# Optimization experiments

Measured on AMD Instinct MI355X. Metric: run time of the kernel, lower is better.

## Reference

```python
import jax, jax.numpy as jnp
import numpy as np

N_HEADS = 16
EPSILON = 0.01
SCORE_SCALE = 1.0
C_CONST = 2.0 + EPSILON


def setup_inputs() -> dict:
    key = jax.random.key(0)
    k1, k2, k3 = jax.random.split(key, 3)
    B, T, D = 2, 2048, 1024
    x = jax.random.normal(k1, (B, T, D), dtype=jnp.float32)
    # torch nn.Linear convention: weight [out_features, in_features], y = x @ W.T
    Wqkv = jax.random.normal(k2, (3 * D, D), dtype=jnp.float32) * (1.0 / np.sqrt(D))
    Wout = jax.random.normal(k3, (D, D), dtype=jnp.float32) * (1.0 / np.sqrt(D))
    return {"x": x, "Wqkv": Wqkv, "Wout": Wout}


def reference(x, Wqkv, Wout):
    B, T, D = x.shape
    H = N_HEADS
    hd = D // H
    qkv = x @ Wqkv.T  # [B, T, 3D]
    q, k, v = jnp.split(qkv, 3, axis=-1)
    # [B, H, T, hd]
    q = q.reshape(B, T, H, hd).transpose(0, 2, 1, 3).astype(jnp.float32)
    k = k.reshape(B, T, H, hd).transpose(0, 2, 1, 3).astype(jnp.float32)
    v = v.reshape(B, T, H, hd).transpose(0, 2, 1, 3).astype(jnp.float32)
    # L2 normalize along head dim (F.normalize uses eps=1e-12 via clamp of norm)
    qn = q / jnp.maximum(jnp.linalg.norm(q, axis=-1, keepdims=True), 1e-12)
    kn = k / jnp.maximum(jnp.linalg.norm(k, axis=-1, keepdims=True), 1e-12)
    # full T x T kernel matrix per (batch, head)
    x_dot = jnp.einsum("bhtd,bhsd->bhts", qn, kn)
    denom = jnp.maximum(C_CONST - 2.0 * x_dot, 1e-6)
    K = (x_dot * x_dot) / denom * SCORE_SCALE
    causal = jnp.tril(jnp.ones((T, T), dtype=bool))  # keep lower triangle incl. diag
    K = jnp.where(causal[None, None, :, :], K, 0.0)
    numerator = jnp.einsum("bhts,bhsd->bhtd", K, v)
    denominator = jnp.sum(K, axis=-1, keepdims=True)
    out = numerator / (denominator + 1e-6)
    out = out.transpose(0, 2, 1, 3).reshape(B, T, D)
    return out @ Wout.T
```

## Files before the change

kernel.cpp:

```cpp
#include <hip/hip_runtime.h>
#include <hip/hip_bf16.h>

#define T_SEQ 2048
#define D_MODEL 1024
#define BT 4096
#define QKV_N 3072

typedef __attribute__((ext_vector_type(8))) short bf16x8;
typedef __attribute__((ext_vector_type(4))) short bf16x4;
typedef __attribute__((ext_vector_type(4))) float f32x4;

typedef unsigned int __attribute__((address_space(1))) as1_uint;
typedef unsigned int __attribute__((address_space(3))) as3_uint;

__device__ __forceinline__ unsigned short f2bf(float f) {
    unsigned u = __builtin_bit_cast(unsigned, f);
    u += 0x7fffu + ((u >> 16) & 1u);
    return (unsigned short)(u >> 16);
}
__device__ __forceinline__ float bf2f(unsigned short h) {
    unsigned u = ((unsigned)h) << 16;
    return __builtin_bit_cast(float, u);
}
__device__ __forceinline__ void gload_lds16(const void* g, void* l) {
    __builtin_amdgcn_global_load_lds((const as1_uint*)g, (as3_uint*)l, 16, 0, 0);
}
__device__ __forceinline__ unsigned cvtpk_bf16(float lo, float hi) {
    unsigned r;
    asm("v_cvt_pk_bf16_f32 %0, %1, %2" : "=v"(r) : "v"(lo), "v"(hi));
    return r;
}

__global__ __launch_bounds__(256) void cvt_bf16_3(const float* __restrict__ s0, unsigned short* __restrict__ d0, int n0,
                                                  const float* __restrict__ s1, unsigned short* __restrict__ d1, int n1,
                                                  const float* __restrict__ s2, unsigned short* __restrict__ d2, int n2) {
    int i = blockIdx.x * 256 + threadIdx.x;
    const float* s; unsigned short* d;
    if (i < n0) { s = s0; d = d0; }
    else if (i < n0 + n1) { i -= n0; s = s1; d = d1; }
    else if (i < n0 + n1 + n2) { i -= n0 + n1; s = s2; d = d2; }
    else return;
    const float4* sp = (const float4*)s + (size_t)i * 2;
    const float4 a = sp[0], b = sp[1];
    uint4 o;
    o.x = (unsigned)f2bf(a.x) | ((unsigned)f2bf(a.y) << 16);
    o.y = (unsigned)f2bf(a.z) | ((unsigned)f2bf(a.w) << 16);
    o.z = (unsigned)f2bf(b.x) | ((unsigned)f2bf(b.y) << 16);
    o.w = (unsigned)f2bf(b.z) | ((unsigned)f2bf(b.w) << 16);
    ((uint4*)d)[i] = o;
}

template<int MODE>
__global__ __launch_bounds__(256) void gemm_bt_mfma(const unsigned short* __restrict__ A,
                                                    const unsigned short* __restrict__ B,
                                                    void* __restrict__ Cout,
                                                    unsigned short* __restrict__ qbp,
                                                    unsigned short* __restrict__ kbp,
                                                    int M, int N, int K) {
    __shared__ unsigned short As[128 * 64];
    __shared__ unsigned short Bs[128 * 64];
    const int tid = threadIdx.x;
    const int w = tid >> 6;
    const int l = tid & 63;
    const int l15 = l & 15, l4 = l >> 4;

    const int nblocks = (M / 128) * (N / 128);
    const int cpx = nblocks >> 3;
    const int id2 = (blockIdx.x & 7) * cpx + (blockIdx.x >> 3);
    const int bm = (id2 & 31) * 128;
    const int bn = (id2 >> 5) * 128;

    const int wm = (w >> 1) * 64, wn = (w & 1) * 64;

    const f32x4 z = {0.f, 0.f, 0.f, 0.f};
    f32x4 acc[4][4];
#pragma unroll
    for (int m = 0; m < 4; ++m)
#pragma unroll
        for (int n = 0; n < 4; ++n) acc[m][n] = z;

    const int lrow = l >> 3;
    const int lslot = (l & 7) ^ (lrow & 7);

    for (int k0 = 0; k0 < K; k0 += 64) {
#pragma unroll
        for (int i = 0; i < 4; ++i) {
            const int row = w * 32 + i * 8 + lrow;
            gload_lds16(A + (size_t)(bm + row) * K + k0 + lslot * 8, As + (w * 4 + i) * 512);
            gload_lds16(B + (size_t)(bn + row) * K + k0 + lslot * 8, Bs + (w * 4 + i) * 512);
        }
        __syncthreads();
        bf16x8 af[4][2], bfr[4][2];
#pragma unroll
        for (int m = 0; m < 4; ++m) {
            const int row = wm + m * 16 + l15;
            af[m][0] = *(const bf16x8*)(As + row * 64 + ((l4 ^ (row & 7)) * 8));
            af[m][1] = *(const bf16x8*)(As + row * 64 + (((4 + l4) ^ (row & 7)) * 8));
        }
#pragma unroll
        for (int n = 0; n < 4; ++n) {
            const int row = wn + n * 16 + l15;
            bfr[n][0] = *(const bf16x8*)(Bs + row * 64 + ((l4 ^ (row & 7)) * 8));
            bfr[n][1] = *(const bf16x8*)(Bs + row * 64 + (((4 + l4) ^ (row & 7)) * 8));
        }
#pragma unroll
        for (int m = 0; m < 4; ++m)
#pragma unroll
            for (int n = 0; n < 4; ++n) {
                acc[m][n] = __builtin_amdgcn_mfma_f32_16x16x32_bf16(af[m][0], bfr[n][0], acc[m][n], 0, 0, 0);
                acc[m][n] = __builtin_amdgcn_mfma_f32_16x16x32_bf16(af[m][1], bfr[n][1], acc[m][n], 0, 0, 0);
            }
        __syncthreads();
    }

    if (MODE == 0) {
#pragma unroll
        for (int m = 0; m < 4; ++m)
#pragma unroll
            for (int n = 0; n < 4; ++n)
#pragma unroll
                for (int r = 0; r < 4; ++r) {
                    const int row = bm + wm + m * 16 + l4 * 4 + r;
                    const int col = bn + wn + n * 16 + l15;
                    ((float*)Cout)[(size_t)row * N + col] = acc[m][n][r];
                }
    } else {
        const int gcol0 = bn + wn;
        const int part = gcol0 >> 10;
        const int h = (gcol0 >> 6) & 15;
        if (part < 2) {
            unsigned short* dst = part ? kbp : qbp;
#pragma unroll
            for (int m = 0; m < 4; ++m)
#pragma unroll
                for (int r = 0; r < 4; ++r) {
                    float ss = 0.f;
#pragma unroll
                    for (int n = 0; n < 4; ++n) ss = fmaf(acc[m][n][r], acc[m][n][r], ss);
                    ss += __shfl_xor(ss, 1);
                    ss += __shfl_xor(ss, 2);
                    ss += __shfl_xor(ss, 4);
                    ss += __shfl_xor(ss, 8);
                    const float sc = 1.0f / fmaxf(sqrtf(ss), 1e-12f);
                    const int row = bm + wm + m * 16 + l4 * 4 + r;
                    const int bh2 = (row >> 11) * 16 + h;
                    unsigned short* pdst = dst + ((size_t)bh2 * T_SEQ + (row & 2047)) * 64 + l15;
#pragma unroll
                    for (int n = 0; n < 4; ++n) pdst[n * 16] = f2bf(acc[m][n][r] * sc);
                }
        } else {
            unsigned short* vrow = (unsigned short*)Cout;
            const int vcol0 = gcol0 - 2048;
#pragma unroll
            for (int m = 0; m < 4; ++m)
#pragma unroll
                for (int n = 0; n < 4; ++n)
#pragma unroll
                    for (int r = 0; r < 4; ++r) {
                        const int row = bm + wm + m * 16 + l4 * 4 + r;
                        vrow[(size_t)row * D_MODEL + vcol0 + n * 16 + l15] = f2bf(acc[m][n][r]);
                    }
        }
    }
}

__global__ __launch_bounds__(256) void v_cvt_T(const unsigned short* __restrict__ vrow,
                                               unsigned short* __restrict__ vbT) {
    __shared__ unsigned short tile[64][72];
    const int bh = blockIdx.y;
    const int b = bh >> 4, h = bh & 15;
    const int t0 = blockIdx.x * 64;
    const int r = threadIdx.x >> 2;
    const int c = (threadIdx.x & 3) * 16;
    const unsigned short* src = vrow + (size_t)(b * T_SEQ + t0 + r) * D_MODEL + h * 64 + c;
    uint4 v0 = *(const uint4*)(src);
    uint4 v1 = *(const uint4*)(src + 8);
    unsigned short tmp[16];
    *(uint4*)tmp = v0;
    *(uint4*)(tmp + 8) = v1;
#pragma unroll
    for (int j = 0; j < 16; ++j) tile[c + j][r] = tmp[j];
    __syncthreads();
    const int d = threadIdx.x >> 2;
    const int tc = (threadIdx.x & 3) * 16;
    const int t5 = tc >> 5, t4 = (tc >> 4) & 1;
    unsigned short* dstrow = vbT + ((size_t)bh * 64 + d) * T_SEQ + t0;
    const int dp = d & 7;
#pragma unroll
    for (int q = 0; q < 4; ++q) {
        unsigned short tmp2[4];
#pragma unroll
        for (int i = 0; i < 4; ++i) tmp2[i] = tile[d][tc + q * 4 + i];
        const int slot = (t5 * 4 + q) ^ dp;
        *(uint2*)(dstrow + slot * 8 + t4 * 4) = *(uint2*)tmp2;
    }
}

#define AT_TS 64

static __device__ const unsigned char task_tab[48] = {
    (15<<1)|0,(16<<1)|0,(17<<1)|0,(18<<1)|0,(19<<1)|0,(20<<1)|0,(21<<1)|0,(22<<1)|0,
    (23<<1)|0,(24<<1)|0,(25<<1)|0,(26<<1)|0,(27<<1)|0,(28<<1)|0,(29<<1)|0,(30<<1)|0,
    (31<<1)|0,(31<<1)|1,
    (14<<1)|0,(30<<1)|1,(13<<1)|0,(29<<1)|1,(12<<1)|0,(28<<1)|1,(11<<1)|0,(27<<1)|1,
    (10<<1)|0,(26<<1)|1,(9<<1)|0,(25<<1)|1,(8<<1)|0,(24<<1)|1,(7<<1)|0,(23<<1)|1,
    (6<<1)|0,(22<<1)|1,(5<<1)|0,(21<<1)|1,(4<<1)|0,(20<<1)|1,(3<<1)|0,(19<<1)|1,
    (2<<1)|0,(18<<1)|1,(1<<1)|0,(17<<1)|1,(0<<1)|0,(16<<1)|1,
};

__global__ __launch_bounds__(256, 4) void attn_mfma(const unsigned short* __restrict__ qb,
                                                    const unsigned short* __restrict__ kb,
                                                    const unsigned short* __restrict__ vbT,
                                                    unsigned short* __restrict__ attnb,
                                                    unsigned short* __restrict__ pnum,
                                                    float* __restrict__ pden) {
    __shared__ unsigned short Ks[2][64 * 64];
    __shared__ unsigned short Vs[2][64 * 64];

    const int tid = threadIdx.x;
    const int w = tid >> 6;
    const int l = tid & 63;
    const int l15 = l & 15, l4 = l >> 4;

    const int id = blockIdx.x;
    const int xcd = id & 7;
    const int wq = id >> 3;
    const int hl = wq & 3;
    const int task = wq >> 2;
    const int bh = xcd * 4 + hl;
    const int tv = task_tab[task];
    const int j = tv >> 1;
    const int chunk = tv & 1;
    const int nst = chunk ? (j - 15) : (j < 16 ? j + 1 : 16);
    const bool mfin = chunk ? true : (j < 16);
    const int s_base = chunk * 16;
    const int t0 = j * 64;

    const size_t hb = (size_t)bh * T_SEQ * 64;

    const int lrow = l >> 3;
    const int lslot = (l & 7) ^ (lrow & 7);
    const unsigned short* kgp[2];
    const unsigned short* vgp[2];
    unsigned short* kdst[2];
    unsigned short* vdst[2];
#pragma unroll
    for (int c = 0; c < 2; ++c) {
        const int row = w * 16 + c * 8 + lrow;
        kgp[c] = kb + hb + (size_t)(s_base * 64 + row) * 64 + lslot * 8;
        vgp[c] = vbT + hb + (size_t)row * T_SEQ + s_base * 64 + (l & 7) * 8;
        kdst[c] = &Ks[0][(w * 2 + c) * 512];
        vdst[c] = &Vs[0][(w * 2 + c) * 512];
    }

    const int p = l15 & 7;
    const unsigned short* kfp0 = &Ks[0][0] + l15 * 64 + ((l4 ^ p) * 8);
    const unsigned short* kfp1 = &Ks[0][0] + l15 * 64 + (((4 + l4) ^ p) * 8);
    const unsigned short* vfp0 = &Vs[0][0] + l15 * 64 + ((l4 ^ p) * 8);
    const unsigned short* vfp1 = &Vs[0][0] + l15 * 64 + (((4 + l4) ^ p) * 8);

    bf16x8 qf0, qf1;
    {
        const unsigned short* qp = qb + hb + (size_t)(t0 + w * 16 + l15) * 64 + l4 * 8;
        qf0 = *(const bf16x8*)(qp);
        qf1 = *(const bf16x8*)(qp + 32);
    }

    const f32x4 z = {0.f, 0.f, 0.f, 0.f};
    f32x4 acc[4];
#pragma unroll
    for (int i = 0; i < 4; ++i) acc[i] = z;
    float accd = 0.f;

    const int wrow0 = t0 + w * 16;
    const int tq = wrow0 + l15;

#pragma unroll
    for (int c = 0; c < 2; ++c) {
        gload_lds16(kgp[c], kdst[c]);
        gload_lds16(vgp[c], vdst[c]);
    }

    auto compute_tile = [&](int roff, int s0, bool mask) {
        const unsigned short* kc0 = kfp0 + roff;
        const unsigned short* kc1 = kfp1 + roff;
        f32x4 sC[4];
        __builtin_amdgcn_s_setprio(1);
#pragma unroll
        for (int sf = 0; sf < 4; ++sf) {
            bf16x8 kf0 = *(const bf16x8*)(kc0 + sf * 1024);
            bf16x8 kf1 = *(const bf16x8*)(kc1 + sf * 1024);
            f32x4 c = z;
            c = __builtin_amdgcn_mfma_f32_16x16x32_bf16(kf0, qf0, c, 0, 0, 0);
            c = __builtin_amdgcn_mfma_f32_16x16x32_bf16(kf1, qf1, c, 0, 0, 0);
            sC[sf] = c;
        }
        __builtin_amdgcn_s_setprio(0);
        float part_ = 0.f;
#pragma unroll
        for (int sf = 0; sf < 4; ++sf)
#pragma unroll
            for (int r = 0; r < 4; ++r) {
                const float xd = sC[sf][r];
                const float den = __builtin_fmaf(-2.0f, xd, 2.01f);
                float Kv = xd * xd * __builtin_amdgcn_rcpf(den);
                if (mask) {
                    const int s = s0 + sf * 16 + l4 * 4 + r;
                    if (s > tq) Kv = 0.f;
                }
                part_ += Kv;
                sC[sf][r] = Kv;
            }
        accd += part_;
        uint4 p0, p1;
        p0.x = cvtpk_bf16(sC[0][0], sC[0][1]);
        p0.y = cvtpk_bf16(sC[0][2], sC[0][3]);
        p0.z = cvtpk_bf16(sC[1][0], sC[1][1]);
        p0.w = cvtpk_bf16(sC[1][2], sC[1][3]);
        p1.x = cvtpk_bf16(sC[2][0], sC[2][1]);
        p1.y = cvtpk_bf16(sC[2][2], sC[2][3]);
        p1.z = cvtpk_bf16(sC[3][0], sC[3][1]);
        p1.w = cvtpk_bf16(sC[3][2], sC[3][3]);
        const bf16x8 a0 = __builtin_bit_cast(bf16x8, p0);
        const bf16x8 a1 = __builtin_bit_cast(bf16x8, p1);
        const unsigned short* vc0 = vfp0 + roff;
        const unsigned short* vc1 = vfp1 + roff;
        __builtin_amdgcn_s_setprio(1);
#pragma unroll
        for (int df = 0; df < 4; ++df) {
            const bf16x8 B0 = *(const bf16x8*)(vc0 + df * 1024);
            const bf16x8 B1 = *(const bf16x8*)(vc1 + df * 1024);
            acc[df] = __builtin_amdgcn_mfma_f32_16x16x32_bf16(a0, B0, acc[df], 0, 0, 0);
            acc[df] = __builtin_amdgcn_mfma_f32_16x16x32_bf16(a1, B1, acc[df], 0, 0, 0);
        }
        __builtin_amdgcn_s_setprio(0);
    };

    for (int st = 0; st < nst - 1; ++st) {
        const int dsto = ((st & 1) ^ 1) * 4096;
#pragma unroll
        for (int c = 0; c < 2; ++c) {
            kgp[c] += 4096;
            vgp[c] += 64;
            gload_lds16(kgp[c], kdst[c] + dsto);
            gload_lds16(vgp[c], vdst[c] + dsto);
        }
        asm volatile("s_waitcnt vmcnt(4)" ::: "memory");
        __builtin_amdgcn_sched_barrier(0);
        __builtin_amdgcn_s_barrier();
        compute_tile((st & 1) * 4096, (s_base + st) * AT_TS, false);
        __builtin_amdgcn_sched_barrier(0);
        __builtin_amdgcn_s_barrier();
    }
    {
        asm volatile("s_waitcnt vmcnt(0)" ::: "memory");
        __builtin_amdgcn_sched_barrier(0);
        __builtin_amdgcn_s_barrier();
        compute_tile(((nst - 1) & 1) * 4096, (s_base + nst - 1) * AT_TS, mfin);
    }

    accd += __shfl_xor(accd, 16);
    accd += __shfl_xor(accd, 32);

    if (!chunk && j < 16) {
        const int b = bh >> 4, h = bh & 15;
#pragma unroll
        for (int r = 0; r < 4; ++r) {
            const float den = __shfl(accd, l4 * 4 + r) + 1e-6f;
#pragma unroll
            for (int df = 0; df < 4; ++df) {
                const int t = wrow0 + l4 * 4 + r;
                const float o = acc[df][r] / den;
                attnb[((size_t)b * T_SEQ + t) * D_MODEL + h * 64 + df * 16 + l15] = f2bf(o);
            }
        }
    } else {
        const int pj = j - 16;
        const int pidx = (bh * 16 + pj) * 2 + chunk;
        unsigned short* np = pnum + (size_t)pidx * 4096;
#pragma unroll
        for (int r = 0; r < 4; ++r)
#pragma unroll
            for (int df = 0; df < 4; ++df)
                np[(w * 16 + l4 * 4 + r) * 64 + df * 16 + l15] = f2bf(acc[df][r]);
        if (l4 == 0) pden[pidx * 64 + w * 16 + l15] = accd;
    }
}

__global__ __launch_bounds__(256) void attn_reduce(const unsigned short* __restrict__ pnum,
                                                   const float* __restrict__ pden,
                                                   unsigned short* __restrict__ attnb) {
    const int bh = blockIdx.y;
    const int jj = blockIdx.x;
    const int row = threadIdx.x >> 2;
    const int d0 = (threadIdx.x & 3) * 16;
    const int pi = (bh * 16 + jj) * 2;
    const float den = pden[pi * 64 + row] + pden[(pi + 1) * 64 + row] + 1e-6f;
    const float inv = 1.0f / den;
    const unsigned short* n0 = pnum + (size_t)pi * 4096 + row * 64 + d0;
    const unsigned short* n1 = n0 + 4096;
    const int b = bh >> 4, h = bh & 15;
    unsigned short* dst = attnb + ((size_t)b * T_SEQ + (16 + jj) * 64 + row) * D_MODEL + h * 64 + d0;
    uint4 a0 = *(const uint4*)n0, a1 = *(const uint4*)(n0 + 8);
    uint4 c0 = *(const uint4*)n1, c1 = *(const uint4*)(n1 + 8);
    unsigned short sa[8], sb[8], o[16];
    *(uint4*)sa = a0; *(uint4*)sb = c0;
#pragma unroll
    for (int i = 0; i < 8; ++i) o[i] = f2bf((bf2f(sa[i]) + bf2f(sb[i])) * inv);
    *(uint4*)sa = a1; *(uint4*)sb = c1;
#pragma unroll
    for (int i = 0; i < 8; ++i) o[8 + i] = f2bf((bf2f(sa[i]) + bf2f(sb[i])) * inv);
    *(uint4*)dst = *(uint4*)o;
    *(uint4*)(dst + 8) = *(uint4*)(o + 8);
}

extern "C" void kernel_launch(void* const* d_in, const int* in_sizes, int n_in,
                              void* d_out, int out_size, void* d_ws, size_t ws_size,
                              hipStream_t stream) {
    const float* x    = (const float*)d_in[0];
    const float* Wqkv = (const float*)d_in[1];
    const float* Wout = (const float*)d_in[2];
    float* out = (float*)d_out;

    char* ws = (char*)d_ws;
    unsigned short* xb    = (unsigned short*)(ws);
    unsigned short* wqkvb = (unsigned short*)(ws + (size_t)8 * 1024 * 1024);
    unsigned short* vrow  = (unsigned short*)(ws + (size_t)16 * 1024 * 1024);
    unsigned short* vbT   = (unsigned short*)(ws + (size_t)24 * 1024 * 1024);
    unsigned short* woutb = (unsigned short*)(ws + (size_t)32 * 1024 * 1024);
    unsigned short* qbp   = (unsigned short*)(ws + (size_t)34 * 1024 * 1024);
    unsigned short* kbp   = (unsigned short*)(ws + (size_t)42 * 1024 * 1024);
    unsigned short* attnb = (unsigned short*)(ws + (size_t)50 * 1024 * 1024);
    unsigned short* pnum  = xb;
    float*          pden  = (float*)vrow;

    cvt_bf16_3<<<4096, 256, 0, stream>>>(x, xb, BT * D_MODEL / 8,
                                         Wqkv, wqkvb, QKV_N * D_MODEL / 8,
                                         Wout, woutb, D_MODEL * D_MODEL / 8);

    gemm_bt_mfma<2><<<(QKV_N / 128) * (BT / 128), 256, 0, stream>>>(
        xb, wqkvb, vrow, qbp, kbp, BT, QKV_N, D_MODEL);

    v_cvt_T<<<dim3(T_SEQ / 64, 32), 256, 0, stream>>>(vrow, vbT);

    attn_mfma<<<1536, 256, 0, stream>>>(qbp, kbp, vbT, attnb, pnum, pden);

    attn_reduce<<<dim3(16, 32), 256, 0, stream>>>(pnum, pden, attnb);

    gemm_bt_mfma<0><<<(D_MODEL / 128) * (BT / 128), 256, 0, stream>>>(
        attnb, woutb, out, nullptr, nullptr, BT, D_MODEL, D_MODEL);
}
```

Before: 175.6 us.

## Fuse V transpose into QKV GEMM epilogue and split attention into three KV chunks

The QKV GEMM epilogue now writes V directly in the transposed, XOR-swizzled bf16 layout the attention kernel reads, which removes the separate v_cvt_T kernel and its round trip through an intermediate row-major buffer. The causal attention work split changes from two 16-tile KV chunks to up to three 11-tile chunks, giving 2016 blocks with more balanced per-block work. The reduce kernel now merges two or three partials. The transposed stores from the GEMM epilogue are strided 8-byte writes, which may coalesce worse, and the extra partials add more reduce traffic.

Result: faster. 169.5 us (-3.5%).

```diff
diff --git a/kernel.cpp b/kernel.cpp
--- a/kernel.cpp
+++ b/kernel.cpp
@@ -127,8 +127,8 @@
     } else {
         const int gcol0 = bn + wn;
         const int part = gcol0 >> 10;
-        const int h = (gcol0 >> 6) & 15;
         if (part < 2) {
+            const int h = (gcol0 >> 6) & 15;
             unsigned short* dst = part ? kbp : qbp;
 #pragma unroll
             for (int m = 0; m < 4; ++m)
@@ -149,63 +149,47 @@
                     for (int n = 0; n < 4; ++n) pdst[n * 16] = f2bf(acc[m][n][r] * sc);
                 }
         } else {
-            unsigned short* vrow = (unsigned short*)Cout;
-            const int vcol0 = gcol0 - 2048;
-#pragma unroll
-            for (int m = 0; m < 4; ++m)
-#pragma unroll
-                for (int n = 0; n < 4; ++n)
-#pragma unroll
-                    for (int r = 0; r < 4; ++r) {
-                        const int row = bm + wm + m * 16 + l4 * 4 + r;
-                        vrow[(size_t)row * D_MODEL + vcol0 + n * 16 + l15] = f2bf(acc[m][n][r]);
-                    }
-        }
-    }
-}
-
-__global__ __launch_bounds__(256) void v_cvt_T(const unsigned short* __restrict__ vrow,
-                                               unsigned short* __restrict__ vbT) {
-    __shared__ unsigned short tile[64][72];
-    const int bh = blockIdx.y;
-    const int b = bh >> 4, h = bh & 15;
-    const int t0 = blockIdx.x * 64;
-    const int r = threadIdx.x >> 2;
-    const int c = (threadIdx.x & 3) * 16;
-    const unsigned short* src = vrow + (size_t)(b * T_SEQ + t0 + r) * D_MODEL + h * 64 + c;
-    uint4 v0 = *(const uint4*)(src);
-    uint4 v1 = *(const uint4*)(src + 8);
-    unsigned short tmp[16];
-    *(uint4*)tmp = v0;
-    *(uint4*)(tmp + 8) = v1;
-#pragma unroll
-    for (int j = 0; j < 16; ++j) tile[c + j][r] = tmp[j];
-    __syncthreads();
-    const int d = threadIdx.x >> 2;
-    const int tc = (threadIdx.x & 3) * 16;
-    const int t5 = tc >> 5, t4 = (tc >> 4) & 1;
-    unsigned short* dstrow = vbT + ((size_t)bh * 64 + d) * T_SEQ + t0;
-    const int dp = d & 7;
-#pragma unroll
-    for (int q = 0; q < 4; ++q) {
-        unsigned short tmp2[4];
-#pragma unroll
-        for (int i = 0; i < 4; ++i) tmp2[i] = tile[d][tc + q * 4 + i];
-        const int slot = (t5 * 4 + q) ^ dp;
-        *(uint2*)(dstrow + slot * 8 + t4 * 4) = *(uint2*)tmp2;
+            unsigned short* vbT = (unsigned short*)Cout;
+            const int b = (bm + wm) >> 11;
+            const int h = ((bn + wn) >> 6) - 32;
+            const int bh2 = b * 16 + h;
+            const int tbase = (bm + wm) & 2047;
+            const int pxor = l15 & 7;
+#pragma unroll
+            for (int n = 0; n < 4; ++n) {
+                unsigned short* dr = vbT + ((size_t)bh2 * 64 + n * 16 + l15) * T_SEQ + tbase;
+#pragma unroll
+                for (int m = 0; m < 4; ++m) {
+                    const int slot = ((m >> 1) * 4 + l4) ^ pxor;
+                    uint2 o;
+                    o.x = cvtpk_bf16(acc[m][n][0], acc[m][n][1]);
+                    o.y = cvtpk_bf16(acc[m][n][2], acc[m][n][3]);
+                    *(uint2*)(dr + slot * 8 + (m & 1) * 4) = o;
+                }
+            }
+        }
     }
 }
 
 #define AT_TS 64
 
-static __device__ const unsigned char task_tab[48] = {
-    (15<<1)|0,(16<<1)|0,(17<<1)|0,(18<<1)|0,(19<<1)|0,(20<<1)|0,(21<<1)|0,(22<<1)|0,
-    (23<<1)|0,(24<<1)|0,(25<<1)|0,(26<<1)|0,(27<<1)|0,(28<<1)|0,(29<<1)|0,(30<<1)|0,
-    (31<<1)|0,(31<<1)|1,
-    (14<<1)|0,(30<<1)|1,(13<<1)|0,(29<<1)|1,(12<<1)|0,(28<<1)|1,(11<<1)|0,(27<<1)|1,
-    (10<<1)|0,(26<<1)|1,(9<<1)|0,(25<<1)|1,(8<<1)|0,(24<<1)|1,(7<<1)|0,(23<<1)|1,
-    (6<<1)|0,(22<<1)|1,(5<<1)|0,(21<<1)|1,(4<<1)|0,(20<<1)|1,(3<<1)|0,(19<<1)|1,
-    (2<<1)|0,(18<<1)|1,(1<<1)|0,(17<<1)|1,(0<<1)|0,(16<<1)|1,
+static __device__ const unsigned char task_tab[63] = {
+    (10<<2)|0,
+    (11<<2)|0,(12<<2)|0,(13<<2)|0,(14<<2)|0,(15<<2)|0,(16<<2)|0,(17<<2)|0,
+    (18<<2)|0,(19<<2)|0,(20<<2)|0,(21<<2)|0,(22<<2)|0,(23<<2)|0,(24<<2)|0,
+    (25<<2)|0,(26<<2)|0,(27<<2)|0,(28<<2)|0,(29<<2)|0,(30<<2)|0,(31<<2)|0,
+    (21<<2)|1,(22<<2)|1,(23<<2)|1,(24<<2)|1,(25<<2)|1,(26<<2)|1,(27<<2)|1,
+    (28<<2)|1,(29<<2)|1,(30<<2)|1,(31<<2)|1,
+    (9<<2)|0,(20<<2)|1,(31<<2)|2,
+    (8<<2)|0,(19<<2)|1,(30<<2)|2,
+    (7<<2)|0,(18<<2)|1,(29<<2)|2,
+    (6<<2)|0,(17<<2)|1,(28<<2)|2,
+    (5<<2)|0,(16<<2)|1,(27<<2)|2,
+    (4<<2)|0,(15<<2)|1,(26<<2)|2,
+    (3<<2)|0,(14<<2)|1,(25<<2)|2,
+    (2<<2)|0,(13<<2)|1,(24<<2)|2,
+    (1<<2)|0,(12<<2)|1,(23<<2)|2,
+    (0<<2)|0,(11<<2)|1,(22<<2)|2,
 };
 
 __global__ __launch_bounds__(256, 4) void attn_mfma(const unsigned short* __restrict__ qb,
@@ -229,11 +213,12 @@
     const int task = wq >> 2;
     const int bh = xcd * 4 + hl;
     const int tv = task_tab[task];
-    const int j = tv >> 1;
-    const int chunk = tv & 1;
-    const int nst = chunk ? (j - 15) : (j < 16 ? j + 1 : 16);
-    const bool mfin = chunk ? true : (j < 16);
-    const int s_base = chunk * 16;
+    const int j = tv >> 2;
+    const int cid = tv & 3;
+    const int s_base = cid * 11;
+    int nst = (cid == 0) ? (j + 1) : (j - s_base + 1);
+    if (nst > 11) nst = 11;
+    const bool mfin = (j <= s_base + 10);
     const int t0 = j * 64;
 
     const size_t hb = (size_t)bh * T_SEQ * 64;
@@ -362,7 +347,7 @@
     accd += __shfl_xor(accd, 16);
     accd += __shfl_xor(accd, 32);
 
-    if (!chunk && j < 16) {
+    if (cid == 0 && j < 11) {
         const int b = bh >> 4, h = bh & 15;
 #pragma unroll
         for (int r = 0; r < 4; ++r) {
@@ -375,8 +360,7 @@
             }
         }
     } else {
-        const int pj = j - 16;
-        const int pidx = (bh * 16 + pj) * 2 + chunk;
+        const int pidx = (bh * 21 + (j - 11)) * 3 + cid;
         unsigned short* np = pnum + (size_t)pidx * 4096;
 #pragma unroll
         for (int r = 0; r < 4; ++r)
@@ -392,24 +376,36 @@
                                                    unsigned short* __restrict__ attnb) {
     const int bh = blockIdx.y;
     const int jj = blockIdx.x;
+    const int j = 11 + jj;
+    const int cnt = (j < 22) ? 2 : 3;
     const int row = threadIdx.x >> 2;
     const int d0 = (threadIdx.x & 3) * 16;
-    const int pi = (bh * 16 + jj) * 2;
-    const float den = pden[pi * 64 + row] + pden[(pi + 1) * 64 + row] + 1e-6f;
-    const float inv = 1.0f / den;
+    const int pi = (bh * 21 + jj) * 3;
+    float den = pden[pi * 64 + row] + pden[(pi + 1) * 64 + row];
+    if (cnt == 3) den += pden[(pi + 2) * 64 + row];
+    const float inv = 1.0f / (den + 1e-6f);
     const unsigned short* n0 = pnum + (size_t)pi * 4096 + row * 64 + d0;
-    const unsigned short* n1 = n0 + 4096;
     const int b = bh >> 4, h = bh & 15;
-    unsigned short* dst = attnb + ((size_t)b * T_SEQ + (16 + jj) * 64 + row) * D_MODEL + h * 64 + d0;
-    uint4 a0 = *(const uint4*)n0, a1 = *(const uint4*)(n0 + 8);
-    uint4 c0 = *(const uint4*)n1, c1 = *(const uint4*)(n1 + 8);
-    unsigned short sa[8], sb[8], o[16];
-    *(uint4*)sa = a0; *(uint4*)sb = c0;
-#pragma unroll
-    for (int i = 0; i < 8; ++i) o[i] = f2bf((bf2f(sa[i]) + bf2f(sb[i])) * inv);
-    *(uint4*)sa = a1; *(uint4*)sb = c1;
-#pragma unroll
-    for (int i = 0; i < 8; ++i) o[8 + i] = f2bf((bf2f(sa[i]) + bf2f(sb[i])) * inv);
+    unsigned short* dst = attnb + ((size_t)b * T_SEQ + j * 64 + row) * D_MODEL + h * 64 + d0;
+    float sum[16];
+    {
+        uint4 a0 = *(const uint4*)n0, a1 = *(const uint4*)(n0 + 8);
+        unsigned short s[16];
+        *(uint4*)s = a0; *(uint4*)(s + 8) = a1;
+#pragma unroll
+        for (int i = 0; i < 16; ++i) sum[i] = bf2f(s[i]);
+    }
+    for (int c = 1; c < cnt; ++c) {
+        const unsigned short* nc = n0 + (size_t)c * 4096;
+        uint4 a0 = *(const uint4*)nc, a1 = *(const uint4*)(nc + 8);
+        unsigned short s[16];
+        *(uint4*)s = a0; *(uint4*)(s + 8) = a1;
+#pragma unroll
+        for (int i = 0; i < 16; ++i) sum[i] += bf2f(s[i]);
+    }
+    unsigned short o[16];
+#pragma unroll
+    for (int i = 0; i < 16; ++i) o[i] = f2bf(sum[i] * inv);
     *(uint4*)dst = *(uint4*)o;
     *(uint4*)(dst + 8) = *(uint4*)(o + 8);
 }
@@ -425,27 +421,24 @@
     char* ws = (char*)d_ws;
     unsigned short* xb    = (unsigned short*)(ws);
     unsigned short* wqkvb = (unsigned short*)(ws + (size_t)8 * 1024 * 1024);
-    unsigned short* vrow  = (unsigned short*)(ws + (size_t)16 * 1024 * 1024);
     unsigned short* vbT   = (unsigned short*)(ws + (size_t)24 * 1024 * 1024);
     unsigned short* woutb = (unsigned short*)(ws + (size_t)32 * 1024 * 1024);
     unsigned short* qbp   = (unsigned short*)(ws + (size_t)34 * 1024 * 1024);
     unsigned short* kbp   = (unsigned short*)(ws + (size_t)42 * 1024 * 1024);
     unsigned short* attnb = (unsigned short*)(ws + (size_t)50 * 1024 * 1024);
     unsigned short* pnum  = xb;
-    float*          pden  = (float*)vrow;
+    float*          pden  = (float*)(ws + (size_t)20 * 1024 * 1024);
 
     cvt_bf16_3<<<4096, 256, 0, stream>>>(x, xb, BT * D_MODEL / 8,
                                          Wqkv, wqkvb, QKV_N * D_MODEL / 8,
                                          Wout, woutb, D_MODEL * D_MODEL / 8);
 
     gemm_bt_mfma<2><<<(QKV_N / 128) * (BT / 128), 256, 0, stream>>>(
-        xb, wqkvb, vrow, qbp, kbp, BT, QKV_N, D_MODEL);
-
-    v_cvt_T<<<dim3(T_SEQ / 64, 32), 256, 0, stream>>>(vrow, vbT);
-
-    attn_mfma<<<1536, 256, 0, stream>>>(qbp, kbp, vbT, attnb, pnum, pden);
-
-    attn_reduce<<<dim3(16, 32), 256, 0, stream>>>(pnum, pden, attnb);
+        xb, wqkvb, vbT, qbp, kbp, BT, QKV_N, D_MODEL);
+
+    attn_mfma<<<2016, 256, 0, stream>>>(qbp, kbp, vbT, attnb, pnum, pden);
+
+    attn_reduce<<<dim3(21, 32), 256, 0, stream>>>(pnum, pden, attnb);
 
     gemm_bt_mfma<0><<<(D_MODEL / 128) * (BT / 128), 256, 0, stream>>>(
         attnb, woutb, out, nullptr, nullptr, BT, D_MODEL, D_MODEL);
```
